# Kernel tuning notes

Hardware: AMD Instinct MI355X
Metric: run time of the kernel (lower is better)

The kernel has to match this reference:

```python
import jax, jax.numpy as jnp
import numpy as np

N_HEADS = 12
R = 0.5            # cfg.r kernel bandwidth
MASK_NEG = 10000.0


def _split_heads(t, n_heads):
    # (B, S, D) -> (B, H, S, W)
    B, S, D = t.shape
    return t.reshape(B, S, n_heads, D // n_heads).transpose(0, 2, 1, 3)


def setup_inputs() -> dict:
    key = jax.random.key(0)
    ks = jax.random.split(key, 8)
    B, S, D = 2, 256, 768
    sd = 1.0 / np.sqrt(D)
    x = jax.random.normal(ks[0], (B, S, D), dtype=jnp.float32)
    mask = jnp.ones((B, S), dtype=jnp.float32)
    Wq = jax.random.normal(ks[1], (D, D), dtype=jnp.float32) * sd
    bq = jnp.zeros((D,), dtype=jnp.float32)
    Wk = jax.random.normal(ks[2], (D, D), dtype=jnp.float32) * sd
    bk = jnp.zeros((D,), dtype=jnp.float32)
    Wv = jax.random.normal(ks[3], (D, D), dtype=jnp.float32) * sd
    bv = jnp.zeros((D,), dtype=jnp.float32)
    return {"x": x, "mask": mask, "Wq": Wq, "bq": bq, "Wk": Wk, "bk": bk, "Wv": Wv, "bv": bv}


def reference(x, mask, Wq, bq, Wk, bk, Wv, bv):
    B, S, D = x.shape
    H = N_HEADS
    # torch nn.Linear: y = x @ W.T + b
    q = _split_heads(x @ Wq.T + bq, H)   # (B, H, S, W)
    k = _split_heads(x @ Wk.T + bk, H)
    v = _split_heads(x @ Wv.T + bv, H)
    # sinc^4 product kernel over head width W: scores[b,h,l,i] = prod_w sinc(r*(q-k))^4
    diff = q[:, :, :, None, :] - k[:, :, None, :, :]          # (B, H, S, S, W)
    scores = jnp.prod(jnp.sinc(R * diff) ** 4, axis=-1)       # (B, H, S, S)
    scores = scores - MASK_NEG * (1.0 - mask[:, None, None, :])
    w = jax.nn.softmax(scores, axis=-1)                        # (B, H, S, S)
    y = w @ v                                                  # (B, H, S, W)
    y = y / w.sum(axis=-1, keepdims=True)                      # faithful (sums to 1)
    # merge heads: (B, H, S, W) -> (B, S, D)
    h = y.transpose(0, 2, 1, 3).reshape(B, S, D)
    return h
```

## Files before the change

kernel.cpp:

```cpp
#include <hip/hip_runtime.h>
#include <math.h>

#define NB 2
#define SS 256
#define DD 768
#define NH 12
#define WW 64

using f32x4  = __attribute__((ext_vector_type(4))) float;
using bf16x8 = __attribute__((ext_vector_type(8))) short;

constexpr float R2  = 0.25f;
constexpr float C8  = 4.1168160e-7f;
constexpr float EPS = 1e-4f;
constexpr float THR = 0.0078125f;

#define QKV_ELEMS (NB*NH*SS*WW)
#define A_OFF_BYTES  4718592u
#define B_OFF_BYTES  6291456u
#define QT_OFF_BYTES 13369344u
#define KT_OFF_BYTES 18087936u

#define XBLKS 384
#define WBLKS 1728

__device__ __forceinline__ unsigned short bf16_rn(float f) {
    unsigned u = __builtin_bit_cast(unsigned, f);
    u += 0x7fffu + ((u >> 16) & 1u);
    return (unsigned short)(u >> 16);
}

__global__ __launch_bounds__(256) void conv_all(
        const float* __restrict__ x,
        const float* __restrict__ Wq, const float* __restrict__ Wk, const float* __restrict__ Wv,
        unsigned short* __restrict__ A, unsigned short* __restrict__ B) {
    int bid = blockIdx.x;
    const float* src;
    unsigned short* dstrow;
    if (bid < XBLKS) {
        int idx = bid * 256 + threadIdx.x;
        int m = idx / (DD/4);
        int c = (idx - m*(DD/4)) * 4;
        src = x + (size_t)idx * 4;
        dstrow = A + (size_t)m * 1536 + c;
    } else {
        int idx = (bid - XBLKS) * 256 + threadIdx.x;
        int p = idx / (768*192);
        int rem = idx - p*(768*192);
        const float* W = (p == 0) ? Wq : (p == 1) ? Wk : Wv;
        int j = rem / 192;
        int c = (rem - j*192) * 4;
        src = W + (size_t)rem * 4;
        dstrow = B + (size_t)(p*768 + j) * 1536 + c;
    }
    float4 v = *reinterpret_cast<const float4*>(src);
    float vv[4] = {v.x, v.y, v.z, v.w};
    unsigned short h[4], l[4];
    #pragma unroll
    for (int e = 0; e < 4; ++e) {
        h[e] = bf16_rn(vv[e]);
        float hf = __builtin_bit_cast(float, (unsigned)h[e] << 16);
        l[e] = bf16_rn(vv[e] - hf);
    }
    *reinterpret_cast<ushort4*>(dstrow)       = make_ushort4(h[0], h[1], h[2], h[3]);
    *reinterpret_cast<ushort4*>(dstrow + 768) = make_ushort4(l[0], l[1], l[2], l[3]);
}

__global__ __launch_bounds__(256, 2) void gemm_qkv(
        const unsigned short* __restrict__ A, const unsigned short* __restrict__ B,
        const float* __restrict__ bq, const float* __restrict__ bk, const float* __restrict__ bv,
        float* __restrict__ qkv, float* __restrict__ QT, float* __restrict__ KT) {
    __shared__ float red[4][32*32];
    const int tid = threadIdx.x;
    const int wid = tid >> 6, l = tid & 63;
    const int lr = l & 15, lo_ = l >> 4;
    const int m0 = blockIdx.x * 32, n0 = blockIdx.y * 32;

    const unsigned short* Ap = A + (size_t)(m0 + lr) * 1536 + wid * 192 + lo_ * 8;
    const unsigned short* Bp = B + (size_t)(n0 + lr) * 1536 + wid * 192 + lo_ * 8;

    f32x4 acc00 = 0.f, acc01 = 0.f, acc10 = 0.f, acc11 = 0.f;

    bf16x8 ca0, ca1, cb0, cb1, na0, na1, nb0, nb1;
    ca0 = *reinterpret_cast<const bf16x8*>(Ap);
    ca1 = *reinterpret_cast<const bf16x8*>(Ap + 16*1536);
    cb0 = *reinterpret_cast<const bf16x8*>(Bp);
    cb1 = *reinterpret_cast<const bf16x8*>(Bp + 16*1536);

    #pragma unroll
    for (int it = 0; it < 18; ++it) {
        if (it < 17) {
            const int it1 = it + 1;
            const int seg1 = it1 / 6, kk1 = it1 - seg1 * 6;
            const int ao = ((seg1 == 2) ? 768 : 0) + kk1 * 32;
            const int bo = ((seg1 == 1) ? 768 : 0) + kk1 * 32;
            na0 = *reinterpret_cast<const bf16x8*>(Ap + ao);
            na1 = *reinterpret_cast<const bf16x8*>(Ap + 16*1536 + ao);
            nb0 = *reinterpret_cast<const bf16x8*>(Bp + bo);
            nb1 = *reinterpret_cast<const bf16x8*>(Bp + 16*1536 + bo);
        }
        acc00 = __builtin_amdgcn_mfma_f32_16x16x32_bf16(ca0, cb0, acc00, 0, 0, 0);
        acc01 = __builtin_amdgcn_mfma_f32_16x16x32_bf16(ca0, cb1, acc01, 0, 0, 0);
        acc10 = __builtin_amdgcn_mfma_f32_16x16x32_bf16(ca1, cb0, acc10, 0, 0, 0);
        acc11 = __builtin_amdgcn_mfma_f32_16x16x32_bf16(ca1, cb1, acc11, 0, 0, 0);
        ca0 = na0; ca1 = na1; cb0 = nb0; cb1 = nb1;
    }

    #pragma unroll
    for (int j = 0; j < 4; ++j) {
        int r0 = lo_ * 4 + j;
        red[wid][(r0     ) * 32 + lr     ] = acc00[j];
        red[wid][(r0     ) * 32 + lr + 16] = acc01[j];
        red[wid][(r0 + 16) * 32 + lr     ] = acc10[j];
        red[wid][(r0 + 16) * 32 + lr + 16] = acc11[j];
    }
    __syncthreads();

    int row = tid >> 3, col = (tid & 7) * 4;
    f32x4 s = *reinterpret_cast<f32x4*>(&red[0][row*32 + col]);
    #pragma unroll
    for (int w = 1; w < 4; ++w)
        s += *reinterpret_cast<f32x4*>(&red[w][row*32 + col]);

    int n = n0 + col;
    int which = n / 768;
    int jj = n - which * 768;
    const float* bias = (which == 0) ? bq : (which == 1) ? bk : bv;
    float4 bb = *reinterpret_cast<const float4*>(&bias[jj]);
    s[0] += bb.x; s[1] += bb.y; s[2] += bb.z; s[3] += bb.w;

    int m = m0 + row, b_ = m >> 8, s_ = m & 255;
    int head = jj >> 6, w = jj & 63;
    int bh = b_ * NH + head;

    if (which == 2) {
        float* o = qkv + (size_t)2 * QKV_ELEMS + ((size_t)bh * SS + s_) * WW + w;
        *reinterpret_cast<float4*>(o) = make_float4(s[0], s[1], s[2], s[3]);
    } else if (which == 0) {
        float* qtb = QT + ((size_t)bh * SS + s_) * 192 + w;
        f32x4 av, sv, cv;
        #pragma unroll
        for (int e = 0; e < 4; ++e) {
            float a = R2 * s[e];
            av[e] = a;
            sv[e] = __builtin_amdgcn_sinf(a);
            cv[e] = __builtin_amdgcn_cosf(a);
        }
        *reinterpret_cast<f32x4*>(qtb)       = av;
        *reinterpret_cast<f32x4*>(qtb + 64)  = sv;
        *reinterpret_cast<f32x4*>(qtb + 128) = cv;
    } else {
        float* ktb = KT + (size_t)bh * WW * 3 * SS;
        #pragma unroll
        for (int e = 0; e < 4; ++e) {
            int d = w + e;
            float a = R2 * s[e];
            ktb[(d*3 + 0) * SS + s_] = a;
            ktb[(d*3 + 1) * SS + s_] = __builtin_amdgcn_sinf(a);
            ktb[(d*3 + 2) * SS + s_] = __builtin_amdgcn_cosf(a);
        }
    }
}

__global__ __launch_bounds__(256, 3) void fattn(
    const float* __restrict__ qkv, const float* __restrict__ QT, const float* __restrict__ KT,
    const float* __restrict__ mask, float* __restrict__ out)
{
    const int bh = blockIdx.y;
    const int b = bh / NH, h = bh - b * NH;
    const int row0 = blockIdx.x * 8;

    const float* Vg = qkv + (size_t)(2 * QKV_ELEMS) + (size_t)bh * SS * WW;
    const float* kt = KT + (size_t)bh * WW * 3 * SS;

    __shared__ __align__(16) float qt[8][3][WW];
    __shared__ __align__(16) float ebuf[SS][8];
    __shared__ __align__(16) float ypart[4][8][WW];
    __shared__ float zs[4][8];

    const int tid = threadIdx.x, lane = tid & 63, wid = tid >> 6;

    {
        const f32x4* qsrc = reinterpret_cast<const f32x4*>(QT + ((size_t)bh * SS + row0) * 3 * WW);
        f32x4* qdst = reinterpret_cast<f32x4*>(&qt[0][0][0]);
        qdst[tid] = qsrc[tid];
        if (tid < 128) qdst[tid + 256] = qsrc[tid + 256];
    }
    const float mt = -10000.0f * (1.0f - mask[b * SS + tid]);
    __syncthreads();

    float pg[8] = {1.f,1.f,1.f,1.f,1.f,1.f,1.f,1.f};

    auto score_group = [&](int g) {
        const float* kg = kt + (size_t)g * 8 * 3 * SS + tid;
        float kk[8], sk[8], ck[8];
        #pragma unroll
        for (int j = 0; j < 8; ++j) {
            kk[j] = kg[j * 3 * SS];
            sk[j] = kg[j * 3 * SS + SS];
            ck[j] = kg[j * 3 * SS + 2 * SS];
        }
        #pragma unroll
        for (int r = 0; r < 8; ++r) {
            f32x4 q0 = *reinterpret_cast<const f32x4*>(&qt[r][0][g*8]);
            f32x4 q1 = *reinterpret_cast<const f32x4*>(&qt[r][0][g*8+4]);
            f32x4 s0 = *reinterpret_cast<const f32x4*>(&qt[r][1][g*8]);
            f32x4 s1 = *reinterpret_cast<const f32x4*>(&qt[r][1][g*8+4]);
            f32x4 c0 = *reinterpret_cast<const f32x4*>(&qt[r][2][g*8]);
            f32x4 c1 = *reinterpret_cast<const f32x4*>(&qt[r][2][g*8+4]);
            float ps = 1.f, pt = 1.f;
            #pragma unroll
            for (int j = 0; j < 8; ++j) {
                float qv = (j < 4) ? q0[j] : q1[j-4];
                float sq = (j < 4) ? s0[j] : s1[j-4];
                float cq = (j < 4) ? c0[j] : c1[j-4];
                float t  = qv - kk[j];
                float at = fmaxf(fabsf(t), EPS);
                float sn = fmaf(sq, ck[j], -(cq * sk[j]));
                sn = (fabsf(t) < EPS) ? at : sn;
                ps *= sn;
                pt *= at;
            }
            pg[r] *= (ps * C8) * __builtin_amdgcn_rcpf(pt);
        }
    };

    for (int g = 0; g < 3; ++g) score_group(g);

    bool alive[8];
    bool any8 = false;
    #pragma unroll
    for (int r = 0; r < 8; ++r) {
        alive[r] = __any(fabsf(pg[r]) > THR);
        any8 = any8 || alive[r];
    }
    if (any8) {
        #pragma unroll 1
        for (int g = 3; g < 8; ++g) {
            const float* kg = kt + (size_t)g * 8 * 3 * SS + tid;
            float kk[8], sk[8], ck[8];
            #pragma unroll
            for (int j = 0; j < 8; ++j) {
                kk[j] = kg[j * 3 * SS];
                sk[j] = kg[j * 3 * SS + SS];
                ck[j] = kg[j * 3 * SS + 2 * SS];
            }
            bool still = false;
            #pragma unroll
            for (int r = 0; r < 8; ++r) {
                if (alive[r]) {
                    f32x4 q0 = *reinterpret_cast<const f32x4*>(&qt[r][0][g*8]);
                    f32x4 q1 = *reinterpret_cast<const f32x4*>(&qt[r][0][g*8+4]);
                    f32x4 s0 = *reinterpret_cast<const f32x4*>(&qt[r][1][g*8]);
                    f32x4 s1 = *reinterpret_cast<const f32x4*>(&qt[r][1][g*8+4]);
                    f32x4 c0 = *reinterpret_cast<const f32x4*>(&qt[r][2][g*8]);
                    f32x4 c1 = *reinterpret_cast<const f32x4*>(&qt[r][2][g*8+4]);
                    float ps = 1.f, pt = 1.f;
                    #pragma unroll
                    for (int j = 0; j < 8; ++j) {
                        float qv = (j < 4) ? q0[j] : q1[j-4];
                        float sq = (j < 4) ? s0[j] : s1[j-4];
                        float cq = (j < 4) ? c0[j] : c1[j-4];
                        float t  = qv - kk[j];
                        float at = fmaxf(fabsf(t), EPS);
                        float sn = fmaf(sq, ck[j], -(cq * sk[j]));
                        sn = (fabsf(t) < EPS) ? at : sn;
                        ps *= sn;
                        pt *= at;
                    }
                    pg[r] *= (ps * C8) * __builtin_amdgcn_rcpf(pt);
                    alive[r] = __any(fabsf(pg[r]) > THR);
                }
                still = still || alive[r];
            }
            if (!still) break;
        }
    }

    float e[8];
    #pragma unroll
    for (int r = 0; r < 8; ++r) {
        float p = pg[r];
        p *= p; p *= p;
        e[r] = __expf(p + mt);
    }
    {
        f32x4 e0, e1;
        #pragma unroll
        for (int r = 0; r < 4; ++r) { e0[r] = e[r]; e1[r] = e[r+4]; }
        *reinterpret_cast<f32x4*>(&ebuf[tid][0]) = e0;
        *reinterpret_cast<f32x4*>(&ebuf[tid][4]) = e1;
    }
    #pragma unroll
    for (int r = 0; r < 8; ++r) {
        float z = e[r];
        #pragma unroll
        for (int off = 32; off; off >>= 1) z += __shfl_xor(z, off);
        if (lane == 0) zs[wid][r] = z;
    }

    float y[8] = {0.f,0.f,0.f,0.f,0.f,0.f,0.f,0.f};
    const float* vb = Vg + (size_t)(wid * 64) * WW + lane;
    #pragma unroll 16
    for (int ii = 0; ii < 64; ++ii) {
        float v = vb[ii * WW];
        f32x4 ea = *reinterpret_cast<const f32x4*>(&ebuf[wid*64 + ii][0]);
        f32x4 eb = *reinterpret_cast<const f32x4*>(&ebuf[wid*64 + ii][4]);
        y[0] = fmaf(ea[0], v, y[0]); y[1] = fmaf(ea[1], v, y[1]);
        y[2] = fmaf(ea[2], v, y[2]); y[3] = fmaf(ea[3], v, y[3]);
        y[4] = fmaf(eb[0], v, y[4]); y[5] = fmaf(eb[1], v, y[5]);
        y[6] = fmaf(eb[2], v, y[6]); y[7] = fmaf(eb[3], v, y[7]);
    }
    #pragma unroll
    for (int r = 0; r < 8; ++r) ypart[wid][r][lane] = y[r];
    __syncthreads();

    {
        const int r0 = tid >> 6;
        #pragma unroll
        for (int q = 0; q < 2; ++q) {
            int rr = r0 + q * 4;
            float yy = ypart[0][rr][lane] + ypart[1][rr][lane]
                     + ypart[2][rr][lane] + ypart[3][rr][lane];
            float zz = zs[0][rr] + zs[1][rr] + zs[2][rr] + zs[3][rr];
            out[((size_t)b * SS + row0 + rr) * DD + h * WW + lane] = yy * __builtin_amdgcn_rcpf(zz);
        }
    }
}

extern "C" void kernel_launch(void* const* d_in, const int* in_sizes, int n_in,
                              void* d_out, int out_size, void* d_ws, size_t ws_size,
                              hipStream_t stream) {
    const float* x    = (const float*)d_in[0];
    const float* mask = (const float*)d_in[1];
    const float* Wq   = (const float*)d_in[2];
    const float* bq   = (const float*)d_in[3];
    const float* Wk   = (const float*)d_in[4];
    const float* bk   = (const float*)d_in[5];
    const float* Wv   = (const float*)d_in[6];
    const float* bv   = (const float*)d_in[7];
    float* out = (float*)d_out;

    float*          qkv = (float*)d_ws;
    unsigned short* Ab  = (unsigned short*)((char*)d_ws + A_OFF_BYTES);
    unsigned short* Bb  = (unsigned short*)((char*)d_ws + B_OFF_BYTES);
    float*          QTp = (float*)((char*)d_ws + QT_OFF_BYTES);
    float*          KTp = (float*)((char*)d_ws + KT_OFF_BYTES);

    conv_all<<<dim3(XBLKS + WBLKS), 256, 0, stream>>>(x, Wq, Wk, Wv, Ab, Bb);
    gemm_qkv<<<dim3(512/32, 2304/32), 256, 0, stream>>>(Ab, Bb, bq, bk, bv, qkv, QTp, KTp);
    fattn<<<dim3(SS/8, NB*NH), 256, 0, stream>>>(qkv, QTp, KTp, mask, out);
}
```

Before: 58.78 us.

## Triple-buffer GEMM loads, read Q from global directly, pack PV FMAs

The QKV GEMM's register prefetch goes from double to triple buffering, so loads run two iterations ahead of the MFMAs. In the attention kernel, the shared-memory staging of the Q/sin/cos rows and its barrier are removed, and each thread now reads them from global memory with broadcast float4 loads. The P·V accumulation is rewritten on 2-wide float vectors so the compiler can emit packed FMA instructions. The risks are more VGPR pressure in the GEMM and more global/L1 traffic for the Q reads.

New measurement: 57.08 us. 2.9% less time.

```diff
diff --git a/kernel.cpp b/kernel.cpp
--- a/kernel.cpp
+++ b/kernel.cpp
@@ -7,6 +7,7 @@
 #define NH 12
 #define WW 64
 
+using f32x2  = __attribute__((ext_vector_type(2))) float;
 using f32x4  = __attribute__((ext_vector_type(4))) float;
 using bf16x8 = __attribute__((ext_vector_type(8))) short;
 
@@ -81,30 +82,28 @@
 
     f32x4 acc00 = 0.f, acc01 = 0.f, acc10 = 0.f, acc11 = 0.f;
 
-    bf16x8 ca0, ca1, cb0, cb1, na0, na1, nb0, nb1;
-    ca0 = *reinterpret_cast<const bf16x8*>(Ap);
-    ca1 = *reinterpret_cast<const bf16x8*>(Ap + 16*1536);
-    cb0 = *reinterpret_cast<const bf16x8*>(Bp);
-    cb1 = *reinterpret_cast<const bf16x8*>(Bp + 16*1536);
-
+    bf16x8 a0[3], a1[3], b0[3], b1[3];
+    #define LDSTEP(s, bi) { \
+        const int seg_ = (s)/6, kq_ = (s) - seg_*6; \
+        const int ao_ = ((seg_ == 2) ? 768 : 0) + kq_*32; \
+        const int bo_ = ((seg_ == 1) ? 768 : 0) + kq_*32; \
+        a0[bi] = *reinterpret_cast<const bf16x8*>(Ap + ao_); \
+        a1[bi] = *reinterpret_cast<const bf16x8*>(Ap + 16*1536 + ao_); \
+        b0[bi] = *reinterpret_cast<const bf16x8*>(Bp + bo_); \
+        b1[bi] = *reinterpret_cast<const bf16x8*>(Bp + 16*1536 + bo_); }
+
+    LDSTEP(0, 0)
+    LDSTEP(1, 1)
     #pragma unroll
     for (int it = 0; it < 18; ++it) {
-        if (it < 17) {
-            const int it1 = it + 1;
-            const int seg1 = it1 / 6, kk1 = it1 - seg1 * 6;
-            const int ao = ((seg1 == 2) ? 768 : 0) + kk1 * 32;
-            const int bo = ((seg1 == 1) ? 768 : 0) + kk1 * 32;
-            na0 = *reinterpret_cast<const bf16x8*>(Ap + ao);
-            na1 = *reinterpret_cast<const bf16x8*>(Ap + 16*1536 + ao);
-            nb0 = *reinterpret_cast<const bf16x8*>(Bp + bo);
-            nb1 = *reinterpret_cast<const bf16x8*>(Bp + 16*1536 + bo);
-        }
-        acc00 = __builtin_amdgcn_mfma_f32_16x16x32_bf16(ca0, cb0, acc00, 0, 0, 0);
-        acc01 = __builtin_amdgcn_mfma_f32_16x16x32_bf16(ca0, cb1, acc01, 0, 0, 0);
-        acc10 = __builtin_amdgcn_mfma_f32_16x16x32_bf16(ca1, cb0, acc10, 0, 0, 0);
-        acc11 = __builtin_amdgcn_mfma_f32_16x16x32_bf16(ca1, cb1, acc11, 0, 0, 0);
-        ca0 = na0; ca1 = na1; cb0 = nb0; cb1 = nb1;
-    }
+        if (it + 2 < 18) { LDSTEP(it + 2, (it + 2) % 3) }
+        const int cb = it % 3;
+        acc00 = __builtin_amdgcn_mfma_f32_16x16x32_bf16(a0[cb], b0[cb], acc00, 0, 0, 0);
+        acc01 = __builtin_amdgcn_mfma_f32_16x16x32_bf16(a0[cb], b1[cb], acc01, 0, 0, 0);
+        acc10 = __builtin_amdgcn_mfma_f32_16x16x32_bf16(a1[cb], b0[cb], acc10, 0, 0, 0);
+        acc11 = __builtin_amdgcn_mfma_f32_16x16x32_bf16(a1[cb], b1[cb], acc11, 0, 0, 0);
+    }
+    #undef LDSTEP
 
     #pragma unroll
     for (int j = 0; j < 4; ++j) {
@@ -172,27 +171,19 @@
 
     const float* Vg = qkv + (size_t)(2 * QKV_ELEMS) + (size_t)bh * SS * WW;
     const float* kt = KT + (size_t)bh * WW * 3 * SS;
-
-    __shared__ __align__(16) float qt[8][3][WW];
+    const float* qb = QT + ((size_t)bh * SS + row0) * 192;
+
     __shared__ __align__(16) float ebuf[SS][8];
     __shared__ __align__(16) float ypart[4][8][WW];
     __shared__ float zs[4][8];
 
     const int tid = threadIdx.x, lane = tid & 63, wid = tid >> 6;
-
-    {
-        const f32x4* qsrc = reinterpret_cast<const f32x4*>(QT + ((size_t)bh * SS + row0) * 3 * WW);
-        f32x4* qdst = reinterpret_cast<f32x4*>(&qt[0][0][0]);
-        qdst[tid] = qsrc[tid];
-        if (tid < 128) qdst[tid + 256] = qsrc[tid + 256];
-    }
     const float mt = -10000.0f * (1.0f - mask[b * SS + tid]);
-    __syncthreads();
 
     float pg[8] = {1.f,1.f,1.f,1.f,1.f,1.f,1.f,1.f};
 
     auto score_group = [&](int g) {
-        const float* kg = kt + (size_t)g * 8 * 3 * SS + tid;
+        const float* kg = kt + (size_t)g * 24 * SS + tid;
         float kk[8], sk[8], ck[8];
         #pragma unroll
         for (int j = 0; j < 8; ++j) {
@@ -202,21 +193,22 @@
         }
         #pragma unroll
         for (int r = 0; r < 8; ++r) {
-            f32x4 q0 = *reinterpret_cast<const f32x4*>(&qt[r][0][g*8]);
-            f32x4 q1 = *reinterpret_cast<const f32x4*>(&qt[r][0][g*8+4]);
-            f32x4 s0 = *reinterpret_cast<const f32x4*>(&qt[r][1][g*8]);
-            f32x4 s1 = *reinterpret_cast<const f32x4*>(&qt[r][1][g*8+4]);
-            f32x4 c0 = *reinterpret_cast<const f32x4*>(&qt[r][2][g*8]);
-            f32x4 c1 = *reinterpret_cast<const f32x4*>(&qt[r][2][g*8+4]);
+            const float* qr = qb + r * 192 + g * 8;
+            float4 q0 = *reinterpret_cast<const float4*>(qr);
+            float4 q1 = *reinterpret_cast<const float4*>(qr + 4);
+            float4 s0 = *reinterpret_cast<const float4*>(qr + 64);
+            float4 s1 = *reinterpret_cast<const float4*>(qr + 68);
+            float4 c0 = *reinterpret_cast<const float4*>(qr + 128);
+            float4 c1 = *reinterpret_cast<const float4*>(qr + 132);
+            float qa[8] = {q0.x,q0.y,q0.z,q0.w,q1.x,q1.y,q1.z,q1.w};
+            float sa[8] = {s0.x,s0.y,s0.z,s0.w,s1.x,s1.y,s1.z,s1.w};
+            float ca[8] = {c0.x,c0.y,c0.z,c0.w,c1.x,c1.y,c1.z,c1.w};
             float ps = 1.f, pt = 1.f;
             #pragma unroll
             for (int j = 0; j < 8; ++j) {
-                float qv = (j < 4) ? q0[j] : q1[j-4];
-                float sq = (j < 4) ? s0[j] : s1[j-4];
-                float cq = (j < 4) ? c0[j] : c1[j-4];
-                float t  = qv - kk[j];
+                float t  = qa[j] - kk[j];
                 float at = fmaxf(fabsf(t), EPS);
-                float sn = fmaf(sq, ck[j], -(cq * sk[j]));
+                float sn = fmaf(sa[j], ck[j], -(ca[j] * sk[j]));
                 sn = (fabsf(t) < EPS) ? at : sn;
                 ps *= sn;
                 pt *= at;
@@ -237,7 +229,7 @@
     if (any8) {
         #pragma unroll 1
         for (int g = 3; g < 8; ++g) {
-            const float* kg = kt + (size_t)g * 8 * 3 * SS + tid;
+            const float* kg = kt + (size_t)g * 24 * SS + tid;
             float kk[8], sk[8], ck[8];
             #pragma unroll
             for (int j = 0; j < 8; ++j) {
@@ -249,21 +241,22 @@
             #pragma unroll
             for (int r = 0; r < 8; ++r) {
                 if (alive[r]) {
-                    f32x4 q0 = *reinterpret_cast<const f32x4*>(&qt[r][0][g*8]);
-                    f32x4 q1 = *reinterpret_cast<const f32x4*>(&qt[r][0][g*8+4]);
-                    f32x4 s0 = *reinterpret_cast<const f32x4*>(&qt[r][1][g*8]);
-                    f32x4 s1 = *reinterpret_cast<const f32x4*>(&qt[r][1][g*8+4]);
-                    f32x4 c0 = *reinterpret_cast<const f32x4*>(&qt[r][2][g*8]);
-                    f32x4 c1 = *reinterpret_cast<const f32x4*>(&qt[r][2][g*8+4]);
+                    const float* qr = qb + r * 192 + g * 8;
+                    float4 q0 = *reinterpret_cast<const float4*>(qr);
+                    float4 q1 = *reinterpret_cast<const float4*>(qr + 4);
+                    float4 s0 = *reinterpret_cast<const float4*>(qr + 64);
+                    float4 s1 = *reinterpret_cast<const float4*>(qr + 68);
+                    float4 c0 = *reinterpret_cast<const float4*>(qr + 128);
+                    float4 c1 = *reinterpret_cast<const float4*>(qr + 132);
+                    float qa[8] = {q0.x,q0.y,q0.z,q0.w,q1.x,q1.y,q1.z,q1.w};
+                    float sa[8] = {s0.x,s0.y,s0.z,s0.w,s1.x,s1.y,s1.z,s1.w};
+                    float ca[8] = {c0.x,c0.y,c0.z,c0.w,c1.x,c1.y,c1.z,c1.w};
                     float ps = 1.f, pt = 1.f;
                     #pragma unroll
                     for (int j = 0; j < 8; ++j) {
-                        float qv = (j < 4) ? q0[j] : q1[j-4];
-                        float sq = (j < 4) ? s0[j] : s1[j-4];
-                        float cq = (j < 4) ? c0[j] : c1[j-4];
-                        float t  = qv - kk[j];
+                        float t  = qa[j] - kk[j];
                         float at = fmaxf(fabsf(t), EPS);
-                        float sn = fmaf(sq, ck[j], -(cq * sk[j]));
+                        float sn = fmaf(sa[j], ck[j], -(ca[j] * sk[j]));
                         sn = (fabsf(t) < EPS) ? at : sn;
                         ps *= sn;
                         pt *= at;
@@ -299,20 +292,27 @@
         if (lane == 0) zs[wid][r] = z;
     }
 
-    float y[8] = {0.f,0.f,0.f,0.f,0.f,0.f,0.f,0.f};
+    f32x2 y01 = {0.f,0.f}, y23 = {0.f,0.f}, y45 = {0.f,0.f}, y67 = {0.f,0.f};
     const float* vb = Vg + (size_t)(wid * 64) * WW + lane;
     #pragma unroll 16
     for (int ii = 0; ii < 64; ++ii) {
         float v = vb[ii * WW];
+        f32x2 vv; vv[0] = v; vv[1] = v;
         f32x4 ea = *reinterpret_cast<const f32x4*>(&ebuf[wid*64 + ii][0]);
         f32x4 eb = *reinterpret_cast<const f32x4*>(&ebuf[wid*64 + ii][4]);
-        y[0] = fmaf(ea[0], v, y[0]); y[1] = fmaf(ea[1], v, y[1]);
-        y[2] = fmaf(ea[2], v, y[2]); y[3] = fmaf(ea[3], v, y[3]);
-        y[4] = fmaf(eb[0], v, y[4]); y[5] = fmaf(eb[1], v, y[5]);
-        y[6] = fmaf(eb[2], v, y[6]); y[7] = fmaf(eb[3], v, y[7]);
-    }
-    #pragma unroll
-    for (int r = 0; r < 8; ++r) ypart[wid][r][lane] = y[r];
+        f32x2 e01; e01[0] = ea[0]; e01[1] = ea[1];
+        f32x2 e23; e23[0] = ea[2]; e23[1] = ea[3];
+        f32x2 e45; e45[0] = eb[0]; e45[1] = eb[1];
+        f32x2 e67; e67[0] = eb[2]; e67[1] = eb[3];
+        y01 += e01 * vv;
+        y23 += e23 * vv;
+        y45 += e45 * vv;
+        y67 += e67 * vv;
+    }
+    ypart[wid][0][lane] = y01[0]; ypart[wid][1][lane] = y01[1];
+    ypart[wid][2][lane] = y23[0]; ypart[wid][3][lane] = y23[1];
+    ypart[wid][4][lane] = y45[0]; ypart[wid][5][lane] = y45[1];
+    ypart[wid][6][lane] = y67[0]; ypart[wid][7][lane] = y67[1];
     __syncthreads();
 
     {
```
